# Performance work log

Hardware: AMD Instinct MI355X
Metric: run time of the kernel (lower is better)

The kernel has to match this reference:

```python
import jax, jax.numpy as jnp
import numpy as np
import math

N_ENTITIES = 200000
N_ITEMS = 100000
N_REL = 40
DIM = 64
N_HEADS = 2
DK = DIM // N_HEADS
N_EDGES = 1500000
K_EDGES = 256
K_ITEMS = 100


def setup_inputs() -> dict:
    key = jax.random.key(0)
    k1, k2, k3, k4, k5, k6 = jax.random.split(key, 6)
    entity_emb = jax.random.normal(k1, (N_ENTITIES, DIM), jnp.float32) * 0.1
    W_Q = jax.random.normal(k2, (DIM, DIM), jnp.float32) * (1.0 / math.sqrt(DIM))
    relation_emb = jax.random.normal(k3, (N_REL - 1, DIM), jnp.float32) * 0.1
    edge_index = jax.random.randint(k4, (2, N_EDGES), 0, N_ENTITIES, jnp.int32)
    # edge_type in [1, N_REL-1]: code indexes relation_emb[edge_type - 1]
    edge_type = jax.random.randint(k5, (N_EDGES,), 1, N_REL, jnp.int32)
    # uniform(0,1) driving the gumbel noise -log(-log(u)); clipped away from 0
    noise_u = jax.random.uniform(k6, (N_EDGES,), jnp.float32, 1e-9, 1.0)
    return {"entity_emb": entity_emb, "W_Q": W_Q, "relation_emb": relation_emb,
            "noise_u": noise_u, "edge_index": edge_index, "edge_type": edge_type}


def reference(entity_emb, W_Q, relation_emb, noise_u, edge_index, edge_type):
    head, tail = edge_index[0], edge_index[1]
    E = edge_index.shape[1]

    # --- norm_attn_computer (AttnHGCN): per-edge multi-head attention ---
    # project once on nodes, then gather (same math as (emb[head] @ W_Q))
    proj = entity_emb @ W_Q                               # [N, D]
    q = proj[head].reshape(E, N_HEADS, DK)                # [E, H, Dk]
    k = proj[tail].reshape(E, N_HEADS, DK)                # [E, H, Dk]
    rel = relation_emb[edge_type - 1].reshape(E, N_HEADS, DK)
    attn = jnp.sum(q * k * rel, axis=-1) / math.sqrt(DK)  # [E, H]
    edge_attn_logits = attn.mean(axis=-1)                 # [E]

    # scatter_softmax over head nodes, then multiply by head degree (norm)
    seg_max = jax.lax.stop_gradient(
        jax.ops.segment_max(edge_attn_logits, head, num_segments=N_ENTITIES))
    ex = jnp.exp(edge_attn_logits - seg_max[head])
    denom = jax.ops.segment_sum(ex, head, num_segments=N_ENTITIES)
    edge_attn_score = ex / denom[head]
    deg = jax.ops.segment_sum(jnp.ones_like(edge_attn_logits), head,
                              num_segments=N_ENTITIES)
    edge_attn_score = edge_attn_score * deg[head]         # [E]

    # --- attn logit sums per item (head + tail scatter_sum), topk 100 ---
    sum_by_node = (jax.ops.segment_sum(edge_attn_logits, head, num_segments=N_ENTITIES)
                   + jax.ops.segment_sum(edge_attn_logits, tail, num_segments=N_ENTITIES))
    top_items_v, top_attn_items = jax.lax.top_k(sum_by_node[:N_ITEMS], K_ITEMS)

    # --- gumbel-noise injection + edge topk 256 ---
    noisy_score = edge_attn_score + (-jnp.log(-jnp.log(noise_u)))
    topk_v, topk_attn_edge_id = jax.lax.top_k(noisy_score, K_EDGES)

    return (edge_attn_score, topk_v, topk_attn_edge_id, top_items_v, top_attn_items)
```

## Files before the change

kernel.cpp:

```cpp
#include <hip/hip_runtime.h>

#define N_ENTITIES 200000
#define N_ITEMS    100000
#define DIM        64
#define N_EDGES    1500000
#define K_EDGES    256
#define K_ITEMS    100
#define SCALE      0.08838834764831845f

#define CAND_CAP   4096
#define NSCANB     ((N_ENTITIES + 255) / 256)

typedef unsigned long long u64;

__device__ __forceinline__ unsigned fkey(float x) {
    unsigned u = __float_as_uint(x);
    return (u & 0x80000000u) ? ~u : (u | 0x80000000u);
}
__device__ __forceinline__ float funkey(unsigned k) {
    return (k & 0x80000000u) ? __uint_as_float(k & 0x7fffffffu)
                             : __uint_as_float(~k);
}

__device__ __forceinline__ void lds_hist_add(unsigned* h, unsigned bin, bool valid, int lane) {
    bool need = valid;
    for (;;) {
        unsigned long long mask = __ballot(need);
        if (mask == 0ull) break;
        int leader = __ffsll(mask) - 1;
        unsigned lbin = __shfl(bin, leader, 64);
        bool same = need && (bin == lbin);
        unsigned long long grp = __ballot(same);
        if (lane == leader) atomicAdd(&h[lbin], (unsigned)__popcll(grp));
        need = need && !same;
    }
}

__device__ __forceinline__ unsigned select_digit(const unsigned* __restrict__ hist,
                                                 unsigned Keff, unsigned* above) {
    unsigned cum = 0;
    int b = 255;
    for (; b > 0; --b) {
        unsigned hb = hist[b];
        if (cum + hb >= Keff) break;
        cum += hb;
    }
    *above = cum;
    return (unsigned)b;
}

__global__ __launch_bounds__(256) void proj_kernel(const float* __restrict__ emb,
                                                   const float* __restrict__ W,
                                                   float* __restrict__ proj,
                                                   const int* __restrict__ head,
                                                   unsigned* __restrict__ degi,
                                                   unsigned* __restrict__ rank) {
    int e = blockIdx.x * blockDim.x + threadIdx.x;
    unsigned rk = 0;
    bool haveEdge = (e < N_EDGES);
    if (haveEdge) rk = atomicAdd(&degi[head[e]], 1u);

    __shared__ float part[4][16][64];
    const int t = threadIdx.x;
    const int c = t & 63;
    const int q = __builtin_amdgcn_readfirstlane(t >> 6);

    float Wreg[16];
#pragma unroll
    for (int j = 0; j < 16; ++j) Wreg[j] = W[(q * 16 + j) * 64 + c];

    const int base = blockIdx.x * 16;
    const float* erow = emb + (size_t)base * 64 + q * 16;

    float acc[16];
#pragma unroll
    for (int r = 0; r < 16; ++r) acc[r] = 0.f;
#pragma unroll
    for (int r = 0; r < 16; ++r) {
#pragma unroll
        for (int j = 0; j < 16; ++j)
            acc[r] += erow[r * 64 + j] * Wreg[j];
    }
#pragma unroll
    for (int r = 0; r < 16; ++r) part[q][r][c] = acc[r];
    __syncthreads();
#pragma unroll
    for (int it = 0; it < 4; ++it) {
        int oi = t + it * 256;
        int r = oi >> 6, cc = oi & 63;
        float s = part[0][r][cc] + part[1][r][cc] + part[2][r][cc] + part[3][r][cc];
        proj[(size_t)(base + r) * 64 + cc] = s;
    }
    if (haveEdge) rank[e] = rk;
}

__global__ void scan1_kernel(const unsigned* __restrict__ degi, unsigned* __restrict__ start,
                             unsigned* __restrict__ bsum) {
    __shared__ unsigned s[256];
    int t = threadIdx.x, i = blockIdx.x * 256 + t;
    unsigned v = (i < N_ENTITIES) ? degi[i] : 0u;
    s[t] = v;
    __syncthreads();
    for (int off = 1; off < 256; off <<= 1) {
        unsigned x = s[t];
        unsigned y = (t >= off) ? s[t - off] : 0u;
        __syncthreads();
        s[t] = x + y;
        __syncthreads();
    }
    if (i < N_ENTITIES) start[i] = s[t] - v;
    if (t == 255) bsum[blockIdx.x] = s[t];
}

__global__ __launch_bounds__(256) void scan23_kernel(const unsigned* __restrict__ bsum,
                                                     unsigned* __restrict__ start) {
    __shared__ unsigned part[4];
    const int b = blockIdx.x;
    const int t = threadIdx.x;
    unsigned s = 0;
    for (int j = t; j < b; j += 256) s += bsum[j];
#pragma unroll
    for (int off = 1; off < 64; off <<= 1) s += __shfl_xor(s, off, 64);
    if ((t & 63) == 0) part[t >> 6] = s;
    __syncthreads();
    unsigned prefix = part[0] + part[1] + part[2] + part[3];
    int i = b * 256 + t;
    if (i < N_ENTITIES) start[i] += prefix;
}

__global__ void scatter_kernel(const int* __restrict__ head, const int* __restrict__ tail,
                               const int* __restrict__ etype,
                               const unsigned* __restrict__ rank,
                               const unsigned* __restrict__ start,
                               u64* __restrict__ rec) {
    int i = blockIdx.x * blockDim.x + threadIdx.x;
    if (i >= N_EDGES) return;
    unsigned slot = start[head[i]] + rank[i];
    u64 R = ((u64)(unsigned)tail[i] << 27) | ((u64)(unsigned)(etype[i] - 1) << 21) | (u64)(unsigned)i;
    rec[slot] = R;
}

__global__ __launch_bounds__(256) void node_pass(const float4* __restrict__ proj4,
                                                 const float4* __restrict__ rel4,
                                                 const u64* __restrict__ rec,
                                                 const unsigned* __restrict__ start,
                                                 const unsigned* __restrict__ degi,
                                                 float* __restrict__ logits,
                                                 float2* __restrict__ nd,
                                                 float* __restrict__ sumhead,
                                                 float* __restrict__ sumtailR,
                                                 int repMask) {
    unsigned xcd;
    asm volatile("s_getreg_b32 %0, hwreg(HW_REG_XCC_ID)" : "=s"(xcd));
    float* st = sumtailR + (size_t)(xcd & (unsigned)repMask) * N_ITEMS;

    int wave = (blockIdx.x * blockDim.x + threadIdx.x) >> 6;
    int lane = threadIdx.x & 63;
    int slot = lane >> 4, sl = lane & 15;
    unsigned s = start[wave], len = degi[wave];
    float4 ph = proj4[(size_t)wave * 16 + sl];
    float dsum = 0.f, lsum = 0.f;
    for (unsigned k0 = 0; k0 < len; k0 += 8) {
        unsigned ka = k0 + slot, kb = ka + 4;
        bool va = (ka < len), vb = (kb < len);
        u64 Ra = rec[s + (va ? ka : 0u)];
        u64 Rb = rec[s + (vb ? kb : 0u)];
        unsigned ta = (unsigned)(Ra >> 27), ra = ((unsigned)(Ra >> 21)) & 63u;
        unsigned tb = (unsigned)(Rb >> 27), rb = ((unsigned)(Rb >> 21)) & 63u;
        unsigned ea = (unsigned)Ra & 0x1FFFFFu, eb = (unsigned)Rb & 0x1FFFFFu;
        float4 pa = proj4[(size_t)ta * 16 + sl];
        float4 qa = rel4[(size_t)ra * 16 + sl];
        float4 pb = proj4[(size_t)tb * 16 + sl];
        float4 qb = rel4[(size_t)rb * 16 + sl];
        float xa = ph.x * pa.x * qa.x + ph.y * pa.y * qa.y + ph.z * pa.z * qa.z + ph.w * pa.w * qa.w;
        float xb = ph.x * pb.x * qb.x + ph.y * pb.y * qb.y + ph.z * pb.z * qb.z + ph.w * pb.w * qb.w;
        xa += __shfl_xor(xa, 1, 64);  xb += __shfl_xor(xb, 1, 64);
        xa += __shfl_xor(xa, 2, 64);  xb += __shfl_xor(xb, 2, 64);
        xa += __shfl_xor(xa, 4, 64);  xb += __shfl_xor(xb, 4, 64);
        xa += __shfl_xor(xa, 8, 64);  xb += __shfl_xor(xb, 8, 64);
        if (sl == 0) {
            if (va) {
                float lg = xa * SCALE;
                logits[ea] = lg;
                dsum += __expf(lg);
                lsum += lg;
                if (ta < N_ITEMS) atomicAdd(&st[ta], lg);
            }
            if (vb) {
                float lg = xb * SCALE;
                logits[eb] = lg;
                dsum += __expf(lg);
                lsum += lg;
                if (tb < N_ITEMS) atomicAdd(&st[tb], lg);
            }
        }
    }
    dsum += __shfl_xor(dsum, 16, 64);
    dsum += __shfl_xor(dsum, 32, 64);
    lsum += __shfl_xor(lsum, 16, 64);
    lsum += __shfl_xor(lsum, 32, 64);
    if (lane == 0) {
        nd[wave] = make_float2(dsum, (float)len);
        sumhead[wave] = lsum;
    }
}

__global__ void edge_pass3(const float* __restrict__ logits, const int* __restrict__ head,
                           const float2* __restrict__ nd, const float* __restrict__ noise_u,
                           const float* __restrict__ sumhead, const float* __restrict__ sumtailR,
                           int R,
                           float* __restrict__ out_scores, unsigned* __restrict__ keysE,
                           unsigned* __restrict__ keysI, unsigned* __restrict__ hists) {
    __shared__ unsigned hE[256];
    __shared__ unsigned hI[256];
    for (int j = threadIdx.x; j < 256; j += blockDim.x) { hE[j] = 0; hI[j] = 0; }
    __syncthreads();
    int i = blockIdx.x * blockDim.x + threadIdx.x;
    int lane = threadIdx.x & 63;

    unsigned bin = 0;
    bool valid = (i < N_EDGES);
    if (valid) {
        float lg = logits[i];
        float2 dd = nd[head[i]];
        float score = __expf(lg) / dd.x * dd.y;
        out_scores[i] = score;
        float noise = -logf(-logf(noise_u[i]));
        unsigned k = fkey(score + noise);
        keysE[i] = k;
        bin = k >> 24;
    }
    lds_hist_add(hE, bin, valid, lane);

    bin = 0;
    valid = (i < N_ITEMS);
    if (valid) {
        float s = sumhead[i];
        for (int r = 0; r < R; ++r) s += sumtailR[(size_t)r * N_ITEMS + i];
        unsigned k = fkey(s);
        keysI[i] = k;
        bin = k >> 24;
    }
    lds_hist_add(hI, bin, valid, lane);

    __syncthreads();
    for (int j = threadIdx.x; j < 256; j += blockDim.x) {
        unsigned v = hE[j];
        if (v) atomicAdd(&hists[j], v);
        v = hI[j];
        if (v) atomicAdd(&hists[3 * 256 + j], v);
    }
}

__global__ void hist_stage_kernel(const unsigned* __restrict__ keysE,
                                  const unsigned* __restrict__ keysI,
                                  unsigned* __restrict__ hists, int stage) {
    __shared__ unsigned h[256];
    for (int j = threadIdx.x; j < 256; j += blockDim.x) h[j] = 0;
    __syncthreads();
    const int y = blockIdx.y;
    const unsigned* keys = y ? keysI : keysE;
    const int n = y ? N_ITEMS : N_EDGES;
    const unsigned K = y ? K_ITEMS : K_EDGES;
    unsigned* H = hists + (size_t)y * 3 * 256;

    unsigned aboveA, prefix;
    unsigned binA = select_digit(H, K, &aboveA);
    if (stage == 1) {
        prefix = binA;
    } else {
        unsigned aboveB;
        unsigned binB = select_digit(H + 256, K - aboveA, &aboveB);
        prefix = (binA << 8) | binB;
    }
    const int shift = 24 - 8 * stage;
    unsigned* out = H + stage * 256;

    const int lane = threadIdx.x & 63;
    const int stride = gridDim.x * blockDim.x;
    for (int idx = blockIdx.x * blockDim.x + threadIdx.x; idx - lane < n; idx += stride) {
        bool valid = (idx < n);
        unsigned bin = 0;
        if (valid) {
            unsigned k = keys[idx];
            if ((k >> (shift + 8)) != prefix) valid = false;
            bin = (k >> shift) & 0xFFu;
        }
        lds_hist_add(h, bin, valid, lane);
    }
    __syncthreads();
    for (int j = threadIdx.x; j < 256; j += blockDim.x) {
        unsigned v = h[j];
        if (v) atomicAdd(&out[j], v);
    }
}

__global__ void collect_kernel(const unsigned* __restrict__ keysE,
                               const unsigned* __restrict__ keysI,
                               const unsigned* __restrict__ hists,
                               unsigned* __restrict__ counters, unsigned* __restrict__ cand) {
    const int y = blockIdx.y;
    const unsigned* keys = y ? keysI : keysE;
    const int n = y ? N_ITEMS : N_EDGES;
    const unsigned K = y ? K_ITEMS : K_EDGES;
    const unsigned* H = hists + (size_t)y * 3 * 256;
    unsigned aboveA, aboveB, aboveC;
    unsigned binA = select_digit(H, K, &aboveA);
    unsigned binB = select_digit(H + 256, K - aboveA, &aboveB);
    unsigned binC = select_digit(H + 512, K - aboveA - aboveB, &aboveC);
    const unsigned T = ((binA << 16) | (binB << 8) | binC) << 8;
    unsigned* cd = cand + (size_t)y * 2 * CAND_CAP;

    int i = blockIdx.x * blockDim.x + threadIdx.x;
    int stride = gridDim.x * blockDim.x;
    for (; i < n; i += stride) {
        unsigned k = keys[i];
        if (k >= T) {
            unsigned p = atomicAdd(&counters[y], 1u);
            if (p < (unsigned)CAND_CAP) { cd[2 * p] = k; cd[2 * p + 1] = (unsigned)i; }
        }
    }
}

__global__ void final_topk_kernel(const unsigned* __restrict__ cand,
                                  const unsigned* __restrict__ counters,
                                  float* __restrict__ out_topkv, float* __restrict__ out_topki,
                                  float* __restrict__ out_itemv, float* __restrict__ out_itemi) {
    __shared__ unsigned sk[CAND_CAP];
    __shared__ unsigned si[CAND_CAP];
    const int y = blockIdx.x;
    const int K = y ? K_ITEMS : K_EDGES;
    float* outv = y ? out_itemv : out_topkv;
    float* outi = y ? out_itemi : out_topki;
    const unsigned* cd = cand + (size_t)y * 2 * CAND_CAP;
    unsigned m = counters[y];
    if (m > (unsigned)CAND_CAP) m = CAND_CAP;
    for (unsigned i = threadIdx.x; i < m; i += blockDim.x) {
        sk[i] = cd[2 * i];
        si[i] = cd[2 * i + 1];
    }
    __syncthreads();
    for (unsigned i = threadIdx.x; i < m; i += blockDim.x) {
        unsigned ki = sk[i], xi = si[i];
        int r = 0;
        for (unsigned j = 0; j < m; ++j) {
            unsigned kj = sk[j];
            if (kj > ki || (kj == ki && si[j] < xi)) r++;
        }
        if (r < K) {
            outv[r] = funkey(ki);
            outi[r] = (float)xi;
        }
    }
}

extern "C" void kernel_launch(void* const* d_in, const int* in_sizes, int n_in,
                              void* d_out, int out_size, void* d_ws, size_t ws_size,
                              hipStream_t stream) {
    (void)in_sizes; (void)n_in; (void)out_size;
    const float* emb    = (const float*)d_in[0];
    const float* W      = (const float*)d_in[1];
    const float* rel    = (const float*)d_in[2];
    const float* noise  = (const float*)d_in[3];
    const int*   eidx   = (const int*)d_in[4];
    const int*   etype  = (const int*)d_in[5];
    const int* head = eidx;
    const int* tail = eidx + N_EDGES;

    float* out        = (float*)d_out;
    float* out_scores = out;
    float* out_topkv  = out + N_EDGES;
    float* out_topki  = out + N_EDGES + K_EDGES;
    float* out_itemv  = out + N_EDGES + 2 * K_EDGES;
    float* out_itemi  = out + N_EDGES + 2 * K_EDGES + K_ITEMS;

    auto layout_floats = [](int R) -> size_t {
        return (size_t)N_ENTITIES * DIM + N_EDGES + 2 * (size_t)N_EDGES
             + N_ENTITIES + N_ENTITIES + (size_t)R * N_ITEMS
             + 2 * 3 * 256 + 2 + 2 * (size_t)N_ENTITIES + N_ENTITIES
             + 1024 + 2 * 2 * CAND_CAP;
    };
    int R = 8;
    while (R > 1 && ws_size < layout_floats(R) * 4) R >>= 1;

    float* ws = (float*)d_ws;
    size_t o = 0;
    float*    proj    = ws + o;               o += (size_t)N_ENTITIES * DIM;
    unsigned* rank    = (unsigned*)(ws + o);
    float*    logits  = ws + o;               o += N_EDGES;
    u64*      rec     = (u64*)(ws + o);       o += 2 * (size_t)N_EDGES;
    unsigned* keysE   = (unsigned*)rec;
    unsigned* keysI   = keysE + N_EDGES;
    unsigned* start   = (unsigned*)(ws + o);  o += N_ENTITIES;
    unsigned* degi    = (unsigned*)(ws + o);  o += N_ENTITIES;
    float*    sumtailR= ws + o;               o += (size_t)R * N_ITEMS;
    unsigned* hists   = (unsigned*)(ws + o);  o += 2 * 3 * 256;
    unsigned* counters= (unsigned*)(ws + o);  o += 2;
    float2*   nd      = (float2*)(ws + o);    o += 2 * (size_t)N_ENTITIES;
    float*    sumhead = ws + o;               o += N_ENTITIES;
    unsigned* bsum    = (unsigned*)(ws + o);  o += 1024;
    unsigned* cand    = (unsigned*)(ws + o);  o += 2 * 2 * CAND_CAP;

    hipMemsetAsync(degi, 0,
                   ((size_t)N_ENTITIES + (size_t)R * N_ITEMS + 2 * 3 * 256 + 2) * 4, stream);
    hipLaunchKernelGGL(proj_kernel, dim3(12500), dim3(256), 0, stream,
                       emb, W, proj, head, degi, rank);
    hipLaunchKernelGGL(scan1_kernel, dim3(NSCANB), dim3(256), 0, stream, degi, start, bsum);
    hipLaunchKernelGGL(scan23_kernel, dim3(NSCANB), dim3(256), 0, stream, bsum, start);
    hipLaunchKernelGGL(scatter_kernel, dim3((N_EDGES + 255) / 256), dim3(256), 0, stream,
                       head, tail, etype, rank, start, rec);
    hipLaunchKernelGGL(node_pass, dim3(N_ENTITIES / 4), dim3(256), 0, stream,
                       (const float4*)proj, (const float4*)rel, rec, start, degi,
                       logits, nd, sumhead, sumtailR, R - 1);
    hipLaunchKernelGGL(edge_pass3, dim3((N_EDGES + 255) / 256), dim3(256), 0, stream,
                       logits, head, (const float2*)nd, noise, sumhead, sumtailR, R,
                       out_scores, keysE, keysI, hists);
    hipLaunchKernelGGL(hist_stage_kernel, dim3(512, 2), dim3(256), 0, stream,
                       keysE, keysI, hists, 1);
    hipLaunchKernelGGL(hist_stage_kernel, dim3(512, 2), dim3(256), 0, stream,
                       keysE, keysI, hists, 2);
    hipLaunchKernelGGL(collect_kernel, dim3(512, 2), dim3(256), 0, stream,
                       keysE, keysI, hists, counters, cand);
    hipLaunchKernelGGL(final_topk_kernel, dim3(2), dim3(1024), 0, stream,
                       cand, counters, out_topkv, out_topki, out_itemv, out_itemi);
}
```

Baseline: 499.9 us.

## Store node-pass logits in CSR order and unroll edge loop to four records

```diff
diff --git a/kernel.cpp b/kernel.cpp
--- a/kernel.cpp
+++ b/kernel.cpp
@@ -12,6 +12,7 @@
 #define NSCANB     ((N_ENTITIES + 255) / 256)
 
 typedef unsigned long long u64;
+
 
 __device__ __forceinline__ unsigned fkey(float x) {
     unsigned u = __float_as_uint(x);
@@ -130,14 +131,15 @@
 
 __global__ void scatter_kernel(const int* __restrict__ head, const int* __restrict__ tail,
                                const int* __restrict__ etype,
-                               const unsigned* __restrict__ rank,
+                               unsigned* __restrict__ rank,
                                const unsigned* __restrict__ start,
-                               u64* __restrict__ rec) {
+                               u64* __restrict__ rec, int csrMode) {
     int i = blockIdx.x * blockDim.x + threadIdx.x;
     if (i >= N_EDGES) return;
     unsigned slot = start[head[i]] + rank[i];
     u64 R = ((u64)(unsigned)tail[i] << 27) | ((u64)(unsigned)(etype[i] - 1) << 21) | (u64)(unsigned)i;
     rec[slot] = R;
+    if (csrMode) rank[i] = slot;
 }
 
 __global__ __launch_bounds__(256) void node_pass(const float4* __restrict__ proj4,
@@ -145,7 +147,8 @@
                                                  const u64* __restrict__ rec,
                                                  const unsigned* __restrict__ start,
                                                  const unsigned* __restrict__ degi,
-                                                 float* __restrict__ logits,
+                                                 float* __restrict__ logitsOut,
+                                                 int csrMode,
                                                  float2* __restrict__ nd,
                                                  float* __restrict__ sumhead,
                                                  float* __restrict__ sumtailR,
@@ -160,38 +163,67 @@
     unsigned s = start[wave], len = degi[wave];
     float4 ph = proj4[(size_t)wave * 16 + sl];
     float dsum = 0.f, lsum = 0.f;
-    for (unsigned k0 = 0; k0 < len; k0 += 8) {
-        unsigned ka = k0 + slot, kb = ka + 4;
-        bool va = (ka < len), vb = (kb < len);
+    for (unsigned k0 = 0; k0 < len; k0 += 16) {
+        unsigned ka = k0 + slot, kb = ka + 4, kc = ka + 8, kd = ka + 12;
+        bool va = (ka < len), vb = (kb < len), vc = (kc < len), vd = (kd < len);
         u64 Ra = rec[s + (va ? ka : 0u)];
         u64 Rb = rec[s + (vb ? kb : 0u)];
-        unsigned ta = (unsigned)(Ra >> 27), ra = ((unsigned)(Ra >> 21)) & 63u;
-        unsigned tb = (unsigned)(Rb >> 27), rb = ((unsigned)(Rb >> 21)) & 63u;
+        u64 Rc = rec[s + (vc ? kc : 0u)];
+        u64 Rd = rec[s + (vd ? kd : 0u)];
+        unsigned ta = (unsigned)(Ra >> 27), ria = ((unsigned)(Ra >> 21)) & 63u;
+        unsigned tb = (unsigned)(Rb >> 27), rib = ((unsigned)(Rb >> 21)) & 63u;
+        unsigned tc = (unsigned)(Rc >> 27), ric = ((unsigned)(Rc >> 21)) & 63u;
+        unsigned td = (unsigned)(Rd >> 27), rid = ((unsigned)(Rd >> 21)) & 63u;
         unsigned ea = (unsigned)Ra & 0x1FFFFFu, eb = (unsigned)Rb & 0x1FFFFFu;
+        unsigned ec = (unsigned)Rc & 0x1FFFFFu, ed = (unsigned)Rd & 0x1FFFFFu;
         float4 pa = proj4[(size_t)ta * 16 + sl];
-        float4 qa = rel4[(size_t)ra * 16 + sl];
+        float4 qa = rel4[(size_t)ria * 16 + sl];
         float4 pb = proj4[(size_t)tb * 16 + sl];
-        float4 qb = rel4[(size_t)rb * 16 + sl];
+        float4 qb = rel4[(size_t)rib * 16 + sl];
+        float4 pc = proj4[(size_t)tc * 16 + sl];
+        float4 qc = rel4[(size_t)ric * 16 + sl];
+        float4 pd = proj4[(size_t)td * 16 + sl];
+        float4 qd = rel4[(size_t)rid * 16 + sl];
         float xa = ph.x * pa.x * qa.x + ph.y * pa.y * qa.y + ph.z * pa.z * qa.z + ph.w * pa.w * qa.w;
         float xb = ph.x * pb.x * qb.x + ph.y * pb.y * qb.y + ph.z * pb.z * qb.z + ph.w * pb.w * qb.w;
+        float xc = ph.x * pc.x * qc.x + ph.y * pc.y * qc.y + ph.z * pc.z * qc.z + ph.w * pc.w * qc.w;
+        float xd = ph.x * pd.x * qd.x + ph.y * pd.y * qd.y + ph.z * pd.z * qd.z + ph.w * pd.w * qd.w;
         xa += __shfl_xor(xa, 1, 64);  xb += __shfl_xor(xb, 1, 64);
+        xc += __shfl_xor(xc, 1, 64);  xd += __shfl_xor(xd, 1, 64);
         xa += __shfl_xor(xa, 2, 64);  xb += __shfl_xor(xb, 2, 64);
+        xc += __shfl_xor(xc, 2, 64);  xd += __shfl_xor(xd, 2, 64);
         xa += __shfl_xor(xa, 4, 64);  xb += __shfl_xor(xb, 4, 64);
+        xc += __shfl_xor(xc, 4, 64);  xd += __shfl_xor(xd, 4, 64);
         xa += __shfl_xor(xa, 8, 64);  xb += __shfl_xor(xb, 8, 64);
+        xc += __shfl_xor(xc, 8, 64);  xd += __shfl_xor(xd, 8, 64);
         if (sl == 0) {
             if (va) {
                 float lg = xa * SCALE;
-                logits[ea] = lg;
+                logitsOut[csrMode ? (s + ka) : ea] = lg;
                 dsum += __expf(lg);
                 lsum += lg;
                 if (ta < N_ITEMS) atomicAdd(&st[ta], lg);
             }
             if (vb) {
                 float lg = xb * SCALE;
-                logits[eb] = lg;
+                logitsOut[csrMode ? (s + kb) : eb] = lg;
                 dsum += __expf(lg);
                 lsum += lg;
                 if (tb < N_ITEMS) atomicAdd(&st[tb], lg);
+            }
+            if (vc) {
+                float lg = xc * SCALE;
+                logitsOut[csrMode ? (s + kc) : ec] = lg;
+                dsum += __expf(lg);
+                lsum += lg;
+                if (tc < N_ITEMS) atomicAdd(&st[tc], lg);
+            }
+            if (vd) {
+                float lg = xd * SCALE;
+                logitsOut[csrMode ? (s + kd) : ed] = lg;
+                dsum += __expf(lg);
+                lsum += lg;
+                if (td < N_ITEMS) atomicAdd(&st[td], lg);
             }
         }
     }
@@ -205,7 +237,10 @@
     }
 }
 
-__global__ void edge_pass3(const float* __restrict__ logits, const int* __restrict__ head,
+__global__ void edge_pass3(const float* __restrict__ logitsEdge,
+                           const float* __restrict__ logitsCsr,
+                           const unsigned* __restrict__ slotmap, int csrMode,
+                           const int* __restrict__ head,
                            const float2* __restrict__ nd, const float* __restrict__ noise_u,
                            const float* __restrict__ sumhead, const float* __restrict__ sumtailR,
                            int R,
@@ -221,7 +256,7 @@
     unsigned bin = 0;
     bool valid = (i < N_EDGES);
     if (valid) {
-        float lg = logits[i];
+        float lg = csrMode ? logitsCsr[slotmap[i]] : logitsEdge[i];
         float2 dd = nd[head[i]];
         float score = __expf(lg) / dd.x * dd.y;
         out_scores[i] = score;
@@ -374,14 +409,19 @@
     float* out_itemv  = out + N_EDGES + 2 * K_EDGES;
     float* out_itemi  = out + N_EDGES + 2 * K_EDGES + K_ITEMS;
 
-    auto layout_floats = [](int R) -> size_t {
+    auto layout_floats = [](int R, int csr) -> size_t {
         return (size_t)N_ENTITIES * DIM + N_EDGES + 2 * (size_t)N_EDGES
              + N_ENTITIES + N_ENTITIES + (size_t)R * N_ITEMS
              + 2 * 3 * 256 + 2 + 2 * (size_t)N_ENTITIES + N_ENTITIES
-             + 1024 + 2 * 2 * CAND_CAP;
+             + 1024 + 2 * 2 * CAND_CAP + (csr ? (size_t)N_EDGES : 0);
     };
-    int R = 8;
-    while (R > 1 && ws_size < layout_floats(R) * 4) R >>= 1;
+    int R = 8, csr = 1;
+    while (R > 1 && ws_size < layout_floats(R, 1) * 4) R >>= 1;
+    if (ws_size < layout_floats(1, 1) * 4) {
+        csr = 0;
+        R = 8;
+        while (R > 1 && ws_size < layout_floats(R, 0) * 4) R >>= 1;
+    }
 
     float* ws = (float*)d_ws;
     size_t o = 0;
@@ -400,6 +440,9 @@
     float*    sumhead = ws + o;               o += N_ENTITIES;
     unsigned* bsum    = (unsigned*)(ws + o);  o += 1024;
     unsigned* cand    = (unsigned*)(ws + o);  o += 2 * 2 * CAND_CAP;
+    float*    logitsCsr = ws + o;             if (csr) o += N_EDGES;
+
+    float*    nodePassLogits = csr ? logitsCsr : logits;
 
     hipMemsetAsync(degi, 0,
                    ((size_t)N_ENTITIES + (size_t)R * N_ITEMS + 2 * 3 * 256 + 2) * 4, stream);
@@ -408,12 +451,13 @@
     hipLaunchKernelGGL(scan1_kernel, dim3(NSCANB), dim3(256), 0, stream, degi, start, bsum);
     hipLaunchKernelGGL(scan23_kernel, dim3(NSCANB), dim3(256), 0, stream, bsum, start);
     hipLaunchKernelGGL(scatter_kernel, dim3((N_EDGES + 255) / 256), dim3(256), 0, stream,
-                       head, tail, etype, rank, start, rec);
+                       head, tail, etype, rank, start, rec, csr);
     hipLaunchKernelGGL(node_pass, dim3(N_ENTITIES / 4), dim3(256), 0, stream,
                        (const float4*)proj, (const float4*)rel, rec, start, degi,
-                       logits, nd, sumhead, sumtailR, R - 1);
+                       nodePassLogits, csr, nd, sumhead, sumtailR, R - 1);
     hipLaunchKernelGGL(edge_pass3, dim3((N_EDGES + 255) / 256), dim3(256), 0, stream,
-                       logits, head, (const float2*)nd, noise, sumhead, sumtailR, R,
+                       logits, logitsCsr, rank, csr, head, (const float2*)nd, noise,
+                       sumhead, sumtailR, R,
                        out_scores, keysE, keysI, hists);
     hipLaunchKernelGGL(hist_stage_kernel, dim3(512, 2), dim3(256), 0, stream,
                        keysE, keysI, hists, 1);
```

New measurement: 512.9 us. +2.6%, slower.
